# Performance work log

Hardware: AMD Instinct MI355X
Metric: run time of the kernel (lower is better)

Reference implementation:

```python
import jax, jax.numpy as jnp
import numpy as np

D_MODEL = 512
NUM_RULES = 16
BATCH = 4
SEQ = 4096


def setup_inputs() -> dict:
    key = jax.random.key(0)
    ks = jax.random.split(key, 7)
    w_scale = 1.0 / np.sqrt(D_MODEL)  # haiku Linear default truncated-normal scale
    inputs = jax.random.normal(ks[0], (BATCH, SEQ, D_MODEL), dtype=jnp.float32)
    # Stacked per-rule parameters: [num_rules, d_model, d_model] / [num_rules, d_model]
    Wc  = jax.random.normal(ks[1], (NUM_RULES, D_MODEL, D_MODEL), dtype=jnp.float32) * w_scale
    bc  = jnp.zeros((NUM_RULES, D_MODEL), dtype=jnp.float32)
    Wa1 = jax.random.normal(ks[2], (NUM_RULES, D_MODEL, D_MODEL), dtype=jnp.float32) * w_scale
    ba1 = jnp.zeros((NUM_RULES, D_MODEL), dtype=jnp.float32)
    Wa2 = jax.random.normal(ks[3], (NUM_RULES, D_MODEL, D_MODEL), dtype=jnp.float32) * w_scale
    ba2 = jnp.zeros((NUM_RULES, D_MODEL), dtype=jnp.float32)
    return {"inputs": inputs, "Wc": Wc, "bc": bc, "Wa1": Wa1, "ba1": ba1,
            "Wa2": Wa2, "ba2": ba2}


def reference(inputs, Wc, bc, Wa1, ba1, Wa2, ba2):
    """Sum over rules of: (Linear->silu->Linear)(x) * mean_seq(sigmoid(Linear(x))).

    Scan over the 16 rules with an accumulator so peak memory stays O(B*S*D)
    instead of O(R*B*S*D).
    """
    def step(acc, params):
        wc, b_c, wa1, b_a1, wa2, b_a2 = params
        # condition score: [B, 1, D] (mean over seq axis, keepdims)
        cond = jax.nn.sigmoid(jnp.einsum('bsd,de->bse', inputs, wc) + b_c)
        cond = cond.mean(axis=1, keepdims=True)
        # gated MLP action: [B, S, D]
        h = jax.nn.silu(jnp.einsum('bsd,de->bse', inputs, wa1) + b_a1)
        act = jnp.einsum('bsd,de->bse', h, wa2) + b_a2
        return acc + act * cond, None

    acc0 = jnp.zeros_like(inputs)
    out, _ = jax.lax.scan(step, acc0, (Wc, bc, Wa1, ba1, Wa2, ba2))
    return out
```

## Files before the change

### kernel.cpp

```cpp
#include <hip/hip_runtime.h>
#include <stdint.h>

typedef unsigned short u16;
typedef __attribute__((ext_vector_type(8))) short short8;
typedef __attribute__((ext_vector_type(4))) float floatx4;

#define M_TOTAL 16384
#define DM 512
#define NRULES 16
#define BK 64

__device__ __forceinline__ u16 f2bf(float f) {
  uint32_t u = __float_as_uint(f);
  u += 0x7fffu + ((u >> 16) & 1u);
  return (u16)(u >> 16);
}

__device__ __forceinline__ void gld_lds16(const u16* g, u16* l) {
  __builtin_amdgcn_global_load_lds(
      (const __attribute__((address_space(1))) void*)g,
      (__attribute__((address_space(3))) void*)l, 16, 0, 0);
}

__device__ __forceinline__ void stage32x64(const u16* __restrict__ src, int ld,
                                           int r0, int k0, u16* lds, int tid) {
  const int row = tid >> 3, p = tid & 7;
  const int g = p ^ (row & 7);
  gld_lds16(src + (size_t)(r0 + row) * ld + k0 + g * 8, lds + tid * 8);
}


__global__ __launch_bounds__(256) void convert_x(const float* __restrict__ x,
                                                 u16* __restrict__ X,
                                                 float* __restrict__ cond) {
  const int gid = blockIdx.x * 256 + threadIdx.x;
  if (gid < NRULES * 4 * DM) cond[gid] = 0.f;
  const int n4 = M_TOTAL * DM / 4;
  for (int i = gid; i < n4; i += gridDim.x * 256) {
    float4 v = ((const float4*)x)[i];
    ushort4 o;
    o.x = f2bf(v.x); o.y = f2bf(v.y); o.z = f2bf(v.z); o.w = f2bf(v.w);
    ((ushort4*)X)[i] = o;
  }
}

__global__ __launch_bounds__(256) void transpose_w(const float* __restrict__ Wc,
                                                   const float* __restrict__ Wa1,
                                                   const float* __restrict__ Wa2,
                                                   u16* __restrict__ WT) {
  __shared__ u16 tile[64][68];
  const int bx = blockIdx.x;
  const int m = bx >> 6, t = bx & 63;
  const int tr = t >> 3, tc = t & 7;
  const float* src = (m < 16 ? Wc : (m < 32 ? Wa1 : Wa2)) + (size_t)(m & 15) * (DM * DM);
  const int tid = threadIdx.x;
#pragma unroll
  for (int rep = 0; rep < 16; rep++) {
    const int idx = rep * 256 + tid;
    const int kr = idx >> 6, nc = idx & 63;
    tile[kr][nc] = f2bf(src[(size_t)(tr * 64 + kr) * DM + tc * 64 + nc]);
  }
  __syncthreads();
  u16* dst = WT + (size_t)m * (DM * DM);
#pragma unroll
  for (int rep = 0; rep < 16; rep++) {
    const int idx = rep * 256 + tid;
    const int nr = idx >> 6, kc = idx & 63;
    dst[(size_t)(tc * 64 + nr) * DM + tr * 64 + kc] = tile[kc][nr];
  }
}

__global__ __launch_bounds__(256) void scale_w2(const u16* __restrict__ WT,
                                                const float* __restrict__ cond,
                                                u16* __restrict__ W2s,
                                                int ruleBase, int G) {
  const int total = G * 4 * DM * (DM / 8);
  for (int idx = blockIdx.x * 256 + threadIdx.x; idx < total; idx += gridDim.x * 256) {
    const int k8 = idx & 63;
    const int n  = (idx >> 6) & (DM - 1);
    const int gb = idx >> 15;
    const int g = gb >> 2, b = gb & 3, rule = ruleBase + g;
    const float c = cond[((size_t)rule * 4 + b) * DM + n] * (1.0f / 4096.0f);
    const uint4 w = *(const uint4*)&WT[((size_t)(32 + rule)) * DM * DM + (size_t)n * DM + k8 * 8];
    uint4 o;
    {
      uint32_t u;
      u = w.x; o.x = (uint32_t)f2bf(__uint_as_float(u << 16) * c) | ((uint32_t)f2bf(__uint_as_float(u & 0xffff0000u) * c) << 16);
      u = w.y; o.y = (uint32_t)f2bf(__uint_as_float(u << 16) * c) | ((uint32_t)f2bf(__uint_as_float(u & 0xffff0000u) * c) << 16);
      u = w.z; o.z = (uint32_t)f2bf(__uint_as_float(u << 16) * c) | ((uint32_t)f2bf(__uint_as_float(u & 0xffff0000u) * c) << 16);
      u = w.w; o.w = (uint32_t)f2bf(__uint_as_float(u << 16) * c) | ((uint32_t)f2bf(__uint_as_float(u & 0xffff0000u) * c) << 16);
    }
    *(uint4*)&W2s[(size_t)gb * DM * DM + (size_t)n * DM + k8 * 8] = o;
  }
}


__global__ __launch_bounds__(256, 3) void p1_kernel(const u16* __restrict__ X,
                                                    const u16* __restrict__ WT,
                                                    const float* __restrict__ bc,
                                                    const float* __restrict__ ba1,
                                                    float* __restrict__ cond,
                                                    u16* __restrict__ H, int ruleBase) {
  __shared__ __attribute__((aligned(16))) u16 ldsA[128 * 64];
  __shared__ __attribute__((aligned(16))) u16 ldsB[128 * 64];
  const int tid = threadIdx.x;
  const int lane = tid & 63, wid = tid >> 6;
  const int waveM = wid >> 1, waveN = wid & 1;
  const int m0 = blockIdx.x * 128;
  const int nb = blockIdx.y;
  const int z = blockIdx.z;
  const int rule = ruleBase + z;
  const bool is_cond = nb < 4;
  const int n0 = (is_cond ? nb : nb - 4) * 128;
  const u16* B = WT + (size_t)(is_cond ? rule : 16 + rule) * (DM * DM);

  floatx4 acc[4][4];
#pragma unroll
  for (int i = 0; i < 4; i++)
#pragma unroll
    for (int j = 0; j < 4; j++) acc[i][j] = (floatx4)0.0f;

  const int lm = lane & 15, lq = lane >> 4, l7 = lane & 7;

  for (int k0 = 0; k0 < DM; k0 += BK) {
    __syncthreads();
#pragma unroll
    for (int q = 0; q < 4; q++) stage32x64(X, DM, m0 + 32 * q, k0, ldsA + q * 2048, tid);
#pragma unroll
    for (int q = 0; q < 4; q++) stage32x64(B, DM, n0 + 32 * q, k0, ldsB + q * 2048, tid);
    __syncthreads();
#pragma unroll
    for (int t = 0; t < 2; t++) {
      const int co = ((t * 4 + lq) ^ l7) * 8;
      short8 a[4], bb[4];
#pragma unroll
      for (int i = 0; i < 4; i++)
        a[i] = *(const short8*)&ldsA[(waveM * 64 + i * 16 + lm) * 64 + co];
#pragma unroll
      for (int j = 0; j < 4; j++)
        bb[j] = *(const short8*)&ldsB[(waveN * 64 + j * 16 + lm) * 64 + co];
#pragma unroll
      for (int i = 0; i < 4; i++)
#pragma unroll
        for (int j = 0; j < 4; j++)
          acc[i][j] = __builtin_amdgcn_mfma_f32_16x16x32_bf16(a[i], bb[j], acc[i][j], 0, 0, 0);
    }
  }

  if (is_cond) {
    const int b = m0 >> 12;
    float s[4];
#pragma unroll
    for (int j = 0; j < 4; j++) {
      const int col = n0 + waveN * 64 + j * 16 + lm;
      const float bias = bc[rule * DM + col];
      float tsum = 0.f;
#pragma unroll
      for (int i = 0; i < 4; i++)
#pragma unroll
        for (int r = 0; r < 4; r++)
          tsum += __builtin_amdgcn_rcpf(1.0f + __expf(-(acc[i][j][r] + bias)));
      s[j] = tsum;
    }
#pragma unroll
    for (int j = 0; j < 4; j++) {
      s[j] += __shfl_xor(s[j], 16);
      s[j] += __shfl_xor(s[j], 32);
    }
    if (lq == 0) {
#pragma unroll
      for (int j = 0; j < 4; j++) {
        const int col = n0 + waveN * 64 + j * 16 + lm;
        atomicAdd(&cond[((size_t)rule * 4 + b) * DM + col], s[j]);
      }
    }
  } else {
    u16* Hr = H + (size_t)z * M_TOTAL * DM;
#pragma unroll
    for (int i = 0; i < 4; i++)
#pragma unroll
      for (int j = 0; j < 4; j++) {
        const int col = n0 + waveN * 64 + j * 16 + lm;
        const float bias = ba1[rule * DM + col];
#pragma unroll
        for (int r = 0; r < 4; r++) {
          const int row = m0 + waveM * 64 + i * 16 + lq * 4 + r;
          const float v = acc[i][j][r] + bias;
          Hr[(size_t)row * DM + col] = f2bf(v * __builtin_amdgcn_rcpf(1.0f + __expf(-v)));
        }
      }
  }
}


__global__ __launch_bounds__(256, 3) void p2_kernel(const u16* __restrict__ H,
                                                    const u16* __restrict__ W2s,
                                                    const float* __restrict__ ba2,
                                                    const float* __restrict__ cond,
                                                    float* __restrict__ out,
                                                    int ruleBase, int G, int accumulate) {
  __shared__ __attribute__((aligned(16))) u16 ldsA[128 * 64];
  __shared__ __attribute__((aligned(16))) u16 ldsB[128 * 64];
  const int tid = threadIdx.x;
  const int lane = tid & 63, wid = tid >> 6;
  const int waveM = wid >> 1, waveN = wid & 1;
  const int m0 = blockIdx.x * 128;
  const int n0 = blockIdx.y * 128;
  const int b = m0 >> 12;
  const int lm = lane & 15, lq = lane >> 4, l7 = lane & 7;

  floatx4 acc[4][4];
#pragma unroll
  for (int i = 0; i < 4; i++)
#pragma unroll
    for (int j = 0; j < 4; j++) acc[i][j] = (floatx4)0.0f;

  for (int g = 0; g < G; g++) {
    const u16* A = H + (size_t)g * M_TOTAL * DM;
    const u16* Bp = W2s + (size_t)(g * 4 + b) * (DM * DM);
    for (int k0 = 0; k0 < DM; k0 += BK) {
      __syncthreads();
#pragma unroll
      for (int q = 0; q < 4; q++) stage32x64(A, DM, m0 + 32 * q, k0, ldsA + q * 2048, tid);
#pragma unroll
      for (int q = 0; q < 4; q++) stage32x64(Bp, DM, n0 + 32 * q, k0, ldsB + q * 2048, tid);
      __syncthreads();
#pragma unroll
      for (int t = 0; t < 2; t++) {
        const int co = ((t * 4 + lq) ^ l7) * 8;
        short8 a[4], bb[4];
#pragma unroll
        for (int i = 0; i < 4; i++)
          a[i] = *(const short8*)&ldsA[(waveM * 64 + i * 16 + lm) * 64 + co];
#pragma unroll
        for (int j = 0; j < 4; j++)
          bb[j] = *(const short8*)&ldsB[(waveN * 64 + j * 16 + lm) * 64 + co];
#pragma unroll
        for (int i = 0; i < 4; i++)
#pragma unroll
          for (int j = 0; j < 4; j++)
            acc[i][j] = __builtin_amdgcn_mfma_f32_16x16x32_bf16(a[i], bb[j], acc[i][j], 0, 0, 0);
      }
    }
  }

#pragma unroll
  for (int j = 0; j < 4; j++) {
    const int col = n0 + waveN * 64 + j * 16 + lm;
    float bt = 0.f;
    for (int g = 0; g < G; g++) {
      const int rule = ruleBase + g;
      bt += cond[((size_t)rule * 4 + b) * DM + col] * ba2[rule * DM + col];
    }
    bt *= (1.0f / 4096.0f);
#pragma unroll
    for (int i = 0; i < 4; i++)
#pragma unroll
      for (int r = 0; r < 4; r++) {
        const int row = m0 + waveM * 64 + i * 16 + lq * 4 + r;
        const size_t idx = (size_t)row * DM + col;
        const float v = acc[i][j][r] + bt;
        out[idx] = accumulate ? (out[idx] + v) : v;
      }
  }
}


extern "C" void kernel_launch(void* const* d_in, const int* in_sizes, int n_in,
                              void* d_out, int out_size, void* d_ws, size_t ws_size,
                              hipStream_t stream) {
  const float* x   = (const float*)d_in[0];
  const float* Wc  = (const float*)d_in[1];
  const float* bc  = (const float*)d_in[2];
  const float* Wa1 = (const float*)d_in[3];
  const float* ba1 = (const float*)d_in[4];
  const float* Wa2 = (const float*)d_in[5];
  const float* ba2 = (const float*)d_in[6];
  float* out = (float*)d_out;

  char* ws = (char*)d_ws;
  const size_t xBytes = (size_t)M_TOTAL * DM * 2;
  const size_t wtBytes = (size_t)48 * DM * DM * 2;
  const size_t condBytes = (size_t)NRULES * 4 * DM * 4;
  const size_t fixed = xBytes + wtBytes + condBytes;
  const size_t hSlice = (size_t)M_TOTAL * DM * 2;
  const size_t w2sSlice = (size_t)4 * DM * DM * 2;

  int G = 1;
  const int cand[5] = {16, 8, 4, 2, 1};
  for (int i = 0; i < 5; i++) {
    if (fixed + (size_t)cand[i] * (hSlice + w2sSlice) <= ws_size) { G = cand[i]; break; }
  }

  u16* X      = (u16*)ws;
  u16* WT     = (u16*)(ws + xBytes);
  float* cond = (float*)(ws + xBytes + wtBytes);
  u16* W2s    = (u16*)(ws + fixed);
  u16* H      = (u16*)(ws + fixed + (size_t)G * w2sSlice);

  convert_x<<<dim3(2048), dim3(256), 0, stream>>>(x, X, cond);
  transpose_w<<<dim3(48 * 64), dim3(256), 0, stream>>>(Wc, Wa1, Wa2, WT);

  for (int rb = 0; rb < NRULES; rb += G) {
    p1_kernel<<<dim3(128, 8, G), dim3(256), 0, stream>>>(X, WT, bc, ba1, cond, H, rb);
    scale_w2<<<dim3(2048), dim3(256), 0, stream>>>(WT, cond, W2s, rb, G);
    p2_kernel<<<dim3(128, 4), dim3(256), 0, stream>>>(H, W2s, ba2, cond, out, rb, G, rb > 0 ? 1 : 0);
  }
}
```

Measured before the change: 591.6 us.

## Split p2 GEMM reduction over rules across two grid slices with partial-sum buffer

The second-stage GEMM, which reduces over G rules, is split-K along the rule dimension into two z-slices. One slice writes directly to the output with the bias term, and the other writes an fp32 partial buffer that a new elementwise kernel then adds to the output. This doubles the block count of p2 (512 blocks before), which should fill the GPU's compute units better, and the launch bound is raised to 4 blocks per SM. The cost is an extra 32 MB write and read of partials plus one more kernel launch per rule batch.

```diff
diff --git a/kernel.cpp b/kernel.cpp
--- a/kernel.cpp
+++ b/kernel.cpp
@@ -94,6 +94,17 @@
   }
 }
 
+__global__ __launch_bounds__(256) void add_partial(float* __restrict__ out,
+                                                   const float* __restrict__ partial) {
+  const int n4 = M_TOTAL * DM / 4;
+  for (int i = blockIdx.x * 256 + threadIdx.x; i < n4; i += gridDim.x * 256) {
+    float4 o = ((const float4*)out)[i];
+    float4 p = ((const float4*)partial)[i];
+    o.x += p.x; o.y += p.y; o.z += p.z; o.w += p.w;
+    ((float4*)out)[i] = o;
+  }
+}
+
 
 __global__ __launch_bounds__(256, 3) void p1_kernel(const u16* __restrict__ X,
                                                     const u16* __restrict__ WT,
@@ -193,12 +204,14 @@
 }
 
 
-__global__ __launch_bounds__(256, 3) void p2_kernel(const u16* __restrict__ H,
+__global__ __launch_bounds__(256, 4) void p2_kernel(const u16* __restrict__ H,
                                                     const u16* __restrict__ W2s,
                                                     const float* __restrict__ ba2,
                                                     const float* __restrict__ cond,
                                                     float* __restrict__ out,
-                                                    int ruleBase, int G, int accumulate) {
+                                                    float* __restrict__ partial,
+                                                    int ruleBase, int G, int Gh,
+                                                    int accumulate) {
   __shared__ __attribute__((aligned(16))) u16 ldsA[128 * 64];
   __shared__ __attribute__((aligned(16))) u16 ldsB[128 * 64];
   const int tid = threadIdx.x;
@@ -206,6 +219,7 @@
   const int waveM = wid >> 1, waveN = wid & 1;
   const int m0 = blockIdx.x * 128;
   const int n0 = blockIdx.y * 128;
+  const int z = blockIdx.z;
   const int b = m0 >> 12;
   const int lm = lane & 15, lq = lane >> 4, l7 = lane & 7;
 
@@ -215,7 +229,8 @@
 #pragma unroll
     for (int j = 0; j < 4; j++) acc[i][j] = (floatx4)0.0f;
 
-  for (int g = 0; g < G; g++) {
+  const int g0 = z * Gh, g1 = (z == 0) ? Gh : G;
+  for (int g = g0; g < g1; g++) {
     const u16* A = H + (size_t)g * M_TOTAL * DM;
     const u16* Bp = W2s + (size_t)(g * 4 + b) * (DM * DM);
     for (int k0 = 0; k0 < DM; k0 += BK) {
@@ -244,24 +259,38 @@
     }
   }
 
-#pragma unroll
-  for (int j = 0; j < 4; j++) {
-    const int col = n0 + waveN * 64 + j * 16 + lm;
-    float bt = 0.f;
-    for (int g = 0; g < G; g++) {
-      const int rule = ruleBase + g;
-      bt += cond[((size_t)rule * 4 + b) * DM + col] * ba2[rule * DM + col];
-    }
-    bt *= (1.0f / 4096.0f);
-#pragma unroll
-    for (int i = 0; i < 4; i++)
-#pragma unroll
-      for (int r = 0; r < 4; r++) {
-        const int row = m0 + waveM * 64 + i * 16 + lq * 4 + r;
-        const size_t idx = (size_t)row * DM + col;
-        const float v = acc[i][j][r] + bt;
-        out[idx] = accumulate ? (out[idx] + v) : v;
+  if (z == 0) {
+#pragma unroll
+    for (int j = 0; j < 4; j++) {
+      const int col = n0 + waveN * 64 + j * 16 + lm;
+      float bt = 0.f;
+      for (int g = 0; g < G; g++) {
+        const int rule = ruleBase + g;
+        bt += cond[((size_t)rule * 4 + b) * DM + col] * ba2[rule * DM + col];
       }
+      bt *= (1.0f / 4096.0f);
+#pragma unroll
+      for (int i = 0; i < 4; i++)
+#pragma unroll
+        for (int r = 0; r < 4; r++) {
+          const int row = m0 + waveM * 64 + i * 16 + lq * 4 + r;
+          const size_t idx = (size_t)row * DM + col;
+          const float v = acc[i][j][r] + bt;
+          out[idx] = accumulate ? (out[idx] + v) : v;
+        }
+    }
+  } else {
+#pragma unroll
+    for (int j = 0; j < 4; j++) {
+      const int col = n0 + waveN * 64 + j * 16 + lm;
+#pragma unroll
+      for (int i = 0; i < 4; i++)
+#pragma unroll
+        for (int r = 0; r < 4; r++) {
+          const int row = m0 + waveM * 64 + i * 16 + lq * 4 + r;
+          partial[(size_t)row * DM + col] = acc[i][j][r];
+        }
+    }
   }
 }
 
@@ -285,25 +314,33 @@
   const size_t fixed = xBytes + wtBytes + condBytes;
   const size_t hSlice = (size_t)M_TOTAL * DM * 2;
   const size_t w2sSlice = (size_t)4 * DM * DM * 2;
+  const size_t partialBytes = (size_t)M_TOTAL * DM * 4;
 
   int G = 1;
   const int cand[5] = {16, 8, 4, 2, 1};
   for (int i = 0; i < 5; i++) {
     if (fixed + (size_t)cand[i] * (hSlice + w2sSlice) <= ws_size) { G = cand[i]; break; }
   }
+  const size_t used = fixed + (size_t)G * (hSlice + w2sSlice);
+  const bool split = (G >= 2) && (used + partialBytes <= ws_size);
 
   u16* X      = (u16*)ws;
   u16* WT     = (u16*)(ws + xBytes);
   float* cond = (float*)(ws + xBytes + wtBytes);
   u16* W2s    = (u16*)(ws + fixed);
   u16* H      = (u16*)(ws + fixed + (size_t)G * w2sSlice);
+  float* partial = (float*)(ws + used);
 
   convert_x<<<dim3(2048), dim3(256), 0, stream>>>(x, X, cond);
   transpose_w<<<dim3(48 * 64), dim3(256), 0, stream>>>(Wc, Wa1, Wa2, WT);
 
+  const int Gh = split ? G / 2 : G;
   for (int rb = 0; rb < NRULES; rb += G) {
     p1_kernel<<<dim3(128, 8, G), dim3(256), 0, stream>>>(X, WT, bc, ba1, cond, H, rb);
     scale_w2<<<dim3(2048), dim3(256), 0, stream>>>(WT, cond, W2s, rb, G);
-    p2_kernel<<<dim3(128, 4), dim3(256), 0, stream>>>(H, W2s, ba2, cond, out, rb, G, rb > 0 ? 1 : 0);
-  }
-}
+    p2_kernel<<<dim3(128, 4, split ? 2 : 1), dim3(256), 0, stream>>>(
+        H, W2s, ba2, cond, out, partial, rb, G, Gh, rb > 0 ? 1 : 0);
+    if (split)
+      add_partial<<<dim3(2048), dim3(256), 0, stream>>>(out, partial);
+  }
+}
```

Result: slower. 696.3 us (+17.7%).
